# Optimization experiments

Measured on AMD Instinct MI355X. Metric: run time of the kernel, lower is better.

Reference implementation:

```python
import jax, jax.numpy as jnp
import numpy as np
import math

GROUPS = 32
HEADS = 8
EPS = 1e-5


def group_norm(x, w, b):
    B, C, H, W = x.shape
    xg = x.reshape(B, GROUPS, C // GROUPS, H, W)
    mu = xg.mean(axis=(2, 3, 4), keepdims=True)
    var = xg.var(axis=(2, 3, 4), keepdims=True)
    xg = (xg - mu) * jax.lax.rsqrt(var + EPS)
    return xg.reshape(B, C, H, W) * w[None, :, None, None] + b[None, :, None, None]


def setup_inputs() -> dict:
    key = jax.random.key(0)
    ks = jax.random.split(key, 3)
    C = 512
    x = jax.random.normal(ks[0], (4, C, 64, 64), dtype=jnp.float32)
    norm_w = jnp.ones((C,), dtype=jnp.float32)
    norm_b = jnp.zeros((C,), dtype=jnp.float32)
    qkv_w = jax.random.normal(ks[1], (3 * C, C), dtype=jnp.float32) * 0.02
    qkv_b = jnp.zeros((3 * C,), dtype=jnp.float32)
    proj_w = jax.random.normal(ks[2], (C, C), dtype=jnp.float32) * 0.02
    proj_b = jnp.zeros((C,), dtype=jnp.float32)
    return {"x": x, "norm_w": norm_w, "norm_b": norm_b, "qkv_w": qkv_w,
            "qkv_b": qkv_b, "proj_w": proj_w, "proj_b": proj_b}


def reference(x, norm_w, norm_b, qkv_w, qkv_b, proj_w, proj_b):
    B, C, H, W = x.shape
    S = H * W
    head_dim = C // HEADS
    scale = 1.0 / math.sqrt(head_dim)

    h = group_norm(x, norm_w, norm_b)
    # 1x1 conv == pointwise linear over channels
    qkv = jnp.einsum('oc,bchw->bohw', qkv_w, h) + qkv_b[None, :, None, None]
    q, k, v = jnp.split(qkv, 3, axis=1)
    q = q.reshape(B, HEADS, head_dim, S)
    k = k.reshape(B, HEADS, head_dim, S)
    v = v.reshape(B, HEADS, head_dim, S)

    # chunked softmax attention in the original is row-wise softmax, i.e.
    # mathematically identical to full attention over all queries
    attn = jnp.einsum('bhdi,bhdj->bhij', q, k) * scale  # [B,H,S,S]
    attn = jax.nn.softmax(attn, axis=-1)
    out = jnp.einsum('bhij,bhdj->bhdi', attn, v)  # [B,H,d,S]

    out = out.reshape(B, C, H, W)
    out = jnp.einsum('oc,bchw->bohw', proj_w, out) + proj_b[None, :, None, None]
    return out + x
```

## Files before the change

kernel.cpp:

```cpp
#include <hip/hip_runtime.h>
#include <hip/hip_bf16.h>

#define NB 4
#define NC 512
#define NS 4096
#define NH 8
#define HD 64
#define NG 32
#define CPG 16
#define QKC 1024
#define CQF 0.18033688f

typedef __attribute__((ext_vector_type(8))) short bf16x8;
typedef __attribute__((ext_vector_type(4))) float f32x4;
typedef __attribute__((ext_vector_type(16))) float f32x16;

__device__ __forceinline__ unsigned short f2bf(float f) {
  union { float f; unsigned int u; } v; v.f = f;
  unsigned int r = v.u + 0x7FFFu + ((v.u >> 16) & 1u);
  return (unsigned short)(r >> 16);
}

__device__ __forceinline__ unsigned short f2bf_rn(float f) {
  union { __hip_bfloat16 h; unsigned short u; } cv;
  cv.h = __float2bfloat16(f);
  return cv.u;
}

__device__ __forceinline__ void gload16(const unsigned short* g, unsigned short* s) {
  __builtin_amdgcn_global_load_lds(
      (const __attribute__((address_space(1))) unsigned int*)g,
      (__attribute__((address_space(3))) unsigned int*)s, 16, 0, 0);
}

__global__ __launch_bounds__(256) void wprep_k(const float* __restrict__ src,
                                               unsigned short* __restrict__ dst,
                                               int n8, int scale_end8, float scale) {
  int i = blockIdx.x * 256 + threadIdx.x;
  if (i >= n8) return;
  const float4* s = (const float4*)src + (size_t)i * 2;
  float4 a = s[0], b = s[1];
  float sc = (i < scale_end8) ? scale : 1.0f;
  ushort4 u0 = make_ushort4(f2bf_rn(a.x * sc), f2bf_rn(a.y * sc),
                            f2bf_rn(a.z * sc), f2bf_rn(a.w * sc));
  ushort4 u1 = make_ushort4(f2bf_rn(b.x * sc), f2bf_rn(b.y * sc),
                            f2bf_rn(b.z * sc), f2bf_rn(b.w * sc));
  uint4 o;
  o.x = (unsigned)u0.x | ((unsigned)u0.y << 16);
  o.y = (unsigned)u0.z | ((unsigned)u0.w << 16);
  o.z = (unsigned)u1.x | ((unsigned)u1.y << 16);
  o.w = (unsigned)u1.z | ((unsigned)u1.w << 16);
  *((uint4*)dst + i) = o;
}

__global__ __launch_bounds__(256) void gn_stats_k(const float* __restrict__ x,
                                                  float* __restrict__ pstats) {
  int bgq = blockIdx.x;
  const float4* xp = (const float4*)(x + (size_t)bgq * (CPG * NS / 4));
  float s = 0.f, s2 = 0.f;
  #pragma unroll 4
  for (int i = threadIdx.x; i < CPG * NS / 16; i += 256) {
    float4 v = xp[i];
    s  += v.x + v.y + v.z + v.w;
    s2 += v.x * v.x + v.y * v.y + v.z * v.z + v.w * v.w;
  }
  #pragma unroll
  for (int off = 32; off > 0; off >>= 1) {
    s  += __shfl_down(s, off);
    s2 += __shfl_down(s2, off);
  }
  __shared__ float rs[4], rs2[4];
  int wid = threadIdx.x >> 6;
  if ((threadIdx.x & 63) == 0) { rs[wid] = s; rs2[wid] = s2; }
  __syncthreads();
  if (threadIdx.x == 0) {
    pstats[bgq * 2]     = rs[0] + rs[1] + rs[2] + rs[3];
    pstats[bgq * 2 + 1] = rs2[0] + rs2[1] + rs2[2] + rs2[3];
  }
}

__global__ __launch_bounds__(256) void gn_apply_k(const float* __restrict__ x,
                                                  const float* __restrict__ pstats,
                                                  const float* __restrict__ nw,
                                                  const float* __restrict__ nb,
                                                  unsigned short* __restrict__ ht) {
  int st = blockIdx.x, ct = blockIdx.y, b = blockIdx.z;
  int c0 = ct * 64, s0 = st * 64;
  __shared__ unsigned short lds[64][72];
  for (int idx = threadIdx.x; idx < 1024; idx += 256) {
    int row = idx >> 4, c4 = idx & 15;
    int c = c0 + row;
    int gi = (b * NG + (c >> 4)) * 4;
    const float4* pq = (const float4*)(pstats + gi * 2);
    float4 p01 = pq[0], p23 = pq[1];
    float sum = p01.x + p01.z + p23.x + p23.z;
    float ssq = p01.y + p01.w + p23.y + p23.w;
    float inv_n = 1.0f / (CPG * NS);
    float mu = sum * inv_n;
    float var = ssq * inv_n - mu * mu;
    float rstd = rsqrtf(var + 1e-5f);
    float sw = nw[c] * rstd;
    float sb = nb[c] - mu * sw;
    float4 v = *(const float4*)(x + ((size_t)b * NC + c) * NS + s0 + c4 * 4);
    ushort4 u = make_ushort4(f2bf(v.x * sw + sb), f2bf(v.y * sw + sb),
                             f2bf(v.z * sw + sb), f2bf(v.w * sw + sb));
    *(ushort4*)&lds[row][c4 * 4] = u;
  }
  __syncthreads();
  for (int idx = threadIdx.x; idx < 1024; idx += 256) {
    int i = idx >> 4, ch = idx & 15;
    ushort4 u = make_ushort4(lds[ch * 4 + 0][i], lds[ch * 4 + 1][i],
                             lds[ch * 4 + 2][i], lds[ch * 4 + 3][i]);
    *(ushort4*)(ht + ((size_t)b * NS + s0 + i) * NC + c0 + ch * 4) = u;
  }
}

__global__ __launch_bounds__(256) void qkv_gemm_k(const unsigned short* __restrict__ ht,
                                                  const unsigned short* __restrict__ wqb,
                                                  const float* __restrict__ bq,
                                                  unsigned short* __restrict__ qk,
                                                  unsigned short* __restrict__ vt) {
  int b = blockIdx.z;
  int m0 = blockIdx.x * 128, n0 = blockIdx.y * 128;
  __shared__ unsigned short alds[128 * 64];
  __shared__ unsigned short blds[128 * 64];
  const unsigned short* A = ht + (size_t)b * NS * NC;
  int tid = threadIdx.x;
  int l = tid & 63, w = tid >> 6;
  int wr = w >> 1, wc = w & 1;
  int lm = l & 15, lg = l >> 4;
  int lrow = l >> 3, lcb = l & 7;
  f32x4 acc[4][4];
  #pragma unroll
  for (int mi = 0; mi < 4; mi++)
    #pragma unroll
    for (int ni = 0; ni < 4; ni++) acc[mi][ni] = (f32x4){0.f, 0.f, 0.f, 0.f};

  for (int k0 = 0; k0 < NC; k0 += 64) {
    #pragma unroll
    for (int j = 0; j < 4; j++) {
      int row = w * 32 + j * 8 + lrow;
      int scb = lcb ^ (row & 7);
      gload16(A   + (size_t)(m0 + row) * NC + k0 + scb * 8, &alds[(w * 4 + j) * 512]);
      gload16(wqb + (size_t)(n0 + row) * NC + k0 + scb * 8, &blds[(w * 4 + j) * 512]);
    }
    __syncthreads();
    #pragma unroll
    for (int ks = 0; ks < 2; ks++) {
      bf16x8 af[4], bfr[4];
      #pragma unroll
      for (int mi = 0; mi < 4; mi++) {
        int row = wr * 64 + mi * 16 + lm;
        af[mi] = *(const bf16x8*)&alds[((row << 6) + (ks << 5) + (lg << 3)) ^ ((row & 7) << 3)];
      }
      #pragma unroll
      for (int ni = 0; ni < 4; ni++) {
        int row = wc * 64 + ni * 16 + lm;
        bfr[ni] = *(const bf16x8*)&blds[((row << 6) + (ks << 5) + (lg << 3)) ^ ((row & 7) << 3)];
      }
      #pragma unroll
      for (int mi = 0; mi < 4; mi++)
        #pragma unroll
        for (int ni = 0; ni < 4; ni++)
          acc[mi][ni] = __builtin_amdgcn_mfma_f32_16x16x32_bf16(af[mi], bfr[ni], acc[mi][ni], 0, 0, 0);
    }
    __syncthreads();
  }
  if (n0 < QKC) {
    #pragma unroll
    for (int mi = 0; mi < 4; mi++) {
      #pragma unroll
      for (int ni = 0; ni < 4; ni++) {
        int o = n0 + wc * 64 + ni * 16 + lm;
        float bias = bq[o];
        if (o < NC) bias *= CQF;
        #pragma unroll
        for (int q = 0; q < 4; q++) {
          int s = m0 + wr * 64 + mi * 16 + lg * 4 + q;
          qk[((size_t)b * NS + s) * QKC + o] = f2bf(acc[mi][ni][q] + bias);
        }
      }
    }
  } else {
    #pragma unroll
    for (int mi = 0; mi < 4; mi++) {
      int s0 = m0 + wr * 64 + mi * 16 + lg * 4;
      #pragma unroll
      for (int ni = 0; ni < 4; ni++) {
        int o = n0 + wc * 64 + ni * 16 + lm;
        float bias = bq[o];
        int dg = o - QKC;
        ushort4 u = make_ushort4(f2bf(acc[mi][ni][0] + bias), f2bf(acc[mi][ni][1] + bias),
                                 f2bf(acc[mi][ni][2] + bias), f2bf(acc[mi][ni][3] + bias));
        *(ushort4*)(vt + ((size_t)b * NC + dg) * NS + s0) = u;
      }
    }
  }
}

__global__ __launch_bounds__(256) void attn_k(const unsigned short* __restrict__ qk,
                                              const unsigned short* __restrict__ vt,
                                              unsigned short* __restrict__ ob) {
  int qt = blockIdx.x, h = blockIdx.y, b = blockIdx.z;
  int tid = threadIdx.x;
  int l = tid & 63, w = tid >> 6;
  int l31 = l & 31, hi = l >> 5;
  __shared__ unsigned short slds[16384];
  const unsigned short* qkb = qk + (size_t)b * NS * QKC;
  const unsigned short* vtb = vt + ((size_t)b * NC + h * HD) * NS;
  int iw = qt * 128 + w * 32;

  bf16x8 fq[4];
  #pragma unroll
  for (int kk = 0; kk < 4; kk++)
    fq[kk] = *(const bf16x8*)(qkb + (size_t)(iw + l31) * QKC + h * HD + kk * 16 + hi * 8);

  bf16x8 ones;
  #pragma unroll
  for (int e = 0; e < 8; e++) ones[e] = (short)0x3F80;

  int rb = (((l31 << 6) + (hi << 3)) ^ ((l31 & 7) << 3));
  int rbk[4] = { rb, rb ^ 16, rb ^ 32, rb ^ 48 };

  int sr = tid >> 3, sch = (tid & 7) * 8;
  const unsigned short* kp0 = qkb + NC + h * HD + (size_t)sr * QKC + sch;
  const unsigned short* kp1 = kp0 + (size_t)32 * QKC;
  const unsigned short* vp0 = vtb + (size_t)sr * NS + sch;
  const unsigned short* vp1 = vp0 + (size_t)32 * NS;
  int dk0 = (((sr << 6) + sch) ^ ((sr & 7) << 3));
  int dk1 = ((((sr + 32) << 6) + sch) ^ ((sr & 7) << 3));

  f32x16 acc_o0 = {}, acc_o1 = {}, acc_l = {};

  bf16x8 vA[8], vB[8], pA[4], pB[4];
  #pragma unroll
  for (int e = 0; e < 8; e++) vB[e] = (bf16x8){0, 0, 0, 0, 0, 0, 0, 0};
  #pragma unroll
  for (int e = 0; e < 4; e++) pB[e] = (bf16x8){0, 0, 0, 0, 0, 0, 0, 0};

  uint4 rk0 = *(const uint4*)kp0, rk1 = *(const uint4*)kp1;
  uint4 rv0 = *(const uint4*)vp0, rv1 = *(const uint4*)vp1;
  *(uint4*)&slds[dk0] = rk0;        *(uint4*)&slds[dk1] = rk1;
  *(uint4*)&slds[4096 + dk0] = rv0; *(uint4*)&slds[4096 + dk1] = rv1;
  kp0 += (size_t)64 * QKC; kp1 += (size_t)64 * QKC; vp0 += 64; vp1 += 64;
  rk0 = *(const uint4*)kp0; rk1 = *(const uint4*)kp1;
  rv0 = *(const uint4*)vp0; rv1 = *(const uint4*)vp1;
  __syncthreads();

  #define CVTSW(SA, q, DST) {                                                       \
    unsigned X0, X1, Y0, Y1;                                                        \
    asm("v_cvt_pk_bf16_f32 %0, %1, %2" : "=v"(X0) : "v"(SA[q*8+0]), "v"(SA[q*8+1]));\
    asm("v_cvt_pk_bf16_f32 %0, %1, %2" : "=v"(X1) : "v"(SA[q*8+2]), "v"(SA[q*8+3]));\
    asm("v_cvt_pk_bf16_f32 %0, %1, %2" : "=v"(Y0) : "v"(SA[q*8+4]), "v"(SA[q*8+5]));\
    asm("v_cvt_pk_bf16_f32 %0, %1, %2" : "=v"(Y1) : "v"(SA[q*8+6]), "v"(SA[q*8+7]));\
    asm("v_permlane32_swap_b32 %0, %1" : "+v"(X0), "+v"(Y0));                       \
    asm("v_permlane32_swap_b32 %0, %1" : "+v"(X1), "+v"(Y1));                       \
    union { unsigned u[4]; bf16x8 v; } pu = {{X0, X1, Y0, Y1}};                     \
    DST = pu.v; }

  #define TILE(BUF, t, VN, VP, PN, PP) {                                            \
    *(uint4*)&slds[(BUF^1)*8192 + dk0] = rk0;                                       \
    *(uint4*)&slds[(BUF^1)*8192 + dk1] = rk1;                                       \
    *(uint4*)&slds[(BUF^1)*8192 + 4096 + dk0] = rv0;                                \
    *(uint4*)&slds[(BUF^1)*8192 + 4096 + dk1] = rv1;                                \
    if ((t) + 2 < 64) {                                                             \
      kp0 += (size_t)64 * QKC; kp1 += (size_t)64 * QKC; vp0 += 64; vp1 += 64;       \
      rk0 = *(const uint4*)kp0; rk1 = *(const uint4*)kp1;                           \
      rv0 = *(const uint4*)vp0; rv1 = *(const uint4*)vp1;                           \
    }                                                                               \
    const unsigned short* Kr = &slds[(BUF)*8192];                                   \
    const unsigned short* Vr = &slds[(BUF)*8192 + 4096];                            \
    f32x16 sa0 = {}, sa1 = {};                                                      \
    __builtin_amdgcn_s_setprio(1);                                                  \
    _Pragma("unroll")                                                               \
    for (int kk = 0; kk < 4; kk++) {                                                \
      bf16x8 ak = *(const bf16x8*)&Kr[rbk[kk]];                                     \
      sa0 = __builtin_amdgcn_mfma_f32_32x32x16_bf16(ak, fq[kk], sa0, 0, 0, 0);      \
    }                                                                               \
    _Pragma("unroll")                                                               \
    for (int kk = 0; kk < 4; kk++) {                                                \
      bf16x8 ak = *(const bf16x8*)&Kr[rbk[kk] + 2048];                              \
      sa1 = __builtin_amdgcn_mfma_f32_32x32x16_bf16(ak, fq[kk], sa1, 0, 0, 0);      \
    }                                                                               \
    _Pragma("unroll")                                                               \
    for (int kk = 0; kk < 4; kk++) {                                                \
      VN[kk]     = *(const bf16x8*)&Vr[rbk[kk]];                                    \
      VN[kk + 4] = *(const bf16x8*)&Vr[rbk[kk] + 2048];                             \
    }                                                                               \
    _Pragma("unroll")                                                               \
    for (int bq_ = 0; bq_ < 4; bq_++) {                                             \
      acc_l  = __builtin_amdgcn_mfma_f32_32x32x16_bf16(PP[bq_], ones, acc_l, 0, 0, 0);        \
      acc_o0 = __builtin_amdgcn_mfma_f32_32x32x16_bf16(PP[bq_], VP[bq_], acc_o0, 0, 0, 0);    \
      acc_o1 = __builtin_amdgcn_mfma_f32_32x32x16_bf16(PP[bq_], VP[bq_ + 4], acc_o1, 0, 0, 0);\
    }                                                                               \
    __builtin_amdgcn_s_setprio(0);                                                  \
    _Pragma("unroll")                                                               \
    for (int r = 0; r < 16; r++) {                                                  \
      sa0[r] = __builtin_amdgcn_exp2f(sa0[r]);                                      \
      sa1[r] = __builtin_amdgcn_exp2f(sa1[r]);                                      \
    }                                                                               \
    CVTSW(sa0, 0, PN[0]);                                                           \
    CVTSW(sa0, 1, PN[1]);                                                           \
    CVTSW(sa1, 0, PN[2]);                                                           \
    CVTSW(sa1, 1, PN[3]);                                                           \
    __syncthreads(); }

  for (int t = 0; t < 64; t += 2) {
    TILE(0, t,     vA, vB, pA, pB)
    TILE(1, t + 1, vB, vA, pB, pA)
  }
  #undef TILE
  #undef CVTSW

  #pragma unroll
  for (int bq_ = 0; bq_ < 4; bq_++) {
    acc_l  = __builtin_amdgcn_mfma_f32_32x32x16_bf16(pB[bq_], ones, acc_l, 0, 0, 0);
    acc_o0 = __builtin_amdgcn_mfma_f32_32x32x16_bf16(pB[bq_], vB[bq_], acc_o0, 0, 0, 0);
    acc_o1 = __builtin_amdgcn_mfma_f32_32x32x16_bf16(pB[bq_], vB[bq_ + 4], acc_o1, 0, 0, 0);
  }

  #pragma unroll
  for (int r = 0; r < 16; r++) {
    float inv = __builtin_amdgcn_rcpf(acc_l[r]);
    int i = (r & 3) + 8 * (r >> 2) + 4 * hi;
    size_t rowo = ((size_t)b * NS + (iw + i)) * NC + h * HD;
    ob[rowo + l31]      = f2bf_rn(acc_o0[r] * inv);
    ob[rowo + 32 + l31] = f2bf_rn(acc_o1[r] * inv);
  }
}

__global__ __launch_bounds__(256) void proj_gemm_k(const unsigned short* __restrict__ wpb,
                                                   const float* __restrict__ bp,
                                                   const unsigned short* __restrict__ obuf,
                                                   const float* __restrict__ x,
                                                   float* __restrict__ out) {
  int b = blockIdx.z;
  int m0 = blockIdx.x * 128, n0 = blockIdx.y * 128;
  __shared__ unsigned short alds[128 * 64];
  __shared__ unsigned short blds[128 * 64];
  const unsigned short* Bt = obuf + (size_t)b * NS * NC;
  int tid = threadIdx.x;
  int l = tid & 63, w = tid >> 6;
  int wr = w >> 1, wc = w & 1;
  int lm = l & 15, lg = l >> 4;
  int lrow = l >> 3, lcb = l & 7;
  f32x4 acc[4][4];
  #pragma unroll
  for (int mi = 0; mi < 4; mi++)
    #pragma unroll
    for (int ni = 0; ni < 4; ni++) acc[mi][ni] = (f32x4){0.f, 0.f, 0.f, 0.f};

  for (int k0 = 0; k0 < NC; k0 += 64) {
    #pragma unroll
    for (int j = 0; j < 4; j++) {
      int row = w * 32 + j * 8 + lrow;
      int scb = lcb ^ (row & 7);
      gload16(wpb + (size_t)(m0 + row) * NC + k0 + scb * 8, &alds[(w * 4 + j) * 512]);
      gload16(Bt  + (size_t)(n0 + row) * NC + k0 + scb * 8, &blds[(w * 4 + j) * 512]);
    }
    __syncthreads();
    #pragma unroll
    for (int ks = 0; ks < 2; ks++) {
      bf16x8 af[4], bfr[4];
      #pragma unroll
      for (int mi = 0; mi < 4; mi++) {
        int row = wr * 64 + mi * 16 + lm;
        af[mi] = *(const bf16x8*)&alds[((row << 6) + (ks << 5) + (lg << 3)) ^ ((row & 7) << 3)];
      }
      #pragma unroll
      for (int ni = 0; ni < 4; ni++) {
        int row = wc * 64 + ni * 16 + lm;
        bfr[ni] = *(const bf16x8*)&blds[((row << 6) + (ks << 5) + (lg << 3)) ^ ((row & 7) << 3)];
      }
      #pragma unroll
      for (int mi = 0; mi < 4; mi++)
        #pragma unroll
        for (int ni = 0; ni < 4; ni++)
          acc[mi][ni] = __builtin_amdgcn_mfma_f32_16x16x32_bf16(af[mi], bfr[ni], acc[mi][ni], 0, 0, 0);
    }
    __syncthreads();
  }
  #pragma unroll
  for (int mi = 0; mi < 4; mi++) {
    #pragma unroll
    for (int q = 0; q < 4; q++) {
      int o = m0 + wr * 64 + mi * 16 + lg * 4 + q;
      float bias = bp[o];
      #pragma unroll
      for (int ni = 0; ni < 4; ni++) {
        int s = n0 + wc * 64 + ni * 16 + lm;
        size_t idx = ((size_t)b * NC + o) * NS + s;
        out[idx] = acc[mi][ni][q] + bias + x[idx];
      }
    }
  }
}

extern "C" void kernel_launch(void* const* d_in, const int* in_sizes, int n_in,
                              void* d_out, int out_size, void* d_ws, size_t ws_size,
                              hipStream_t stream) {
  const float* x  = (const float*)d_in[0];
  const float* nw = (const float*)d_in[1];
  const float* nb = (const float*)d_in[2];
  const float* wq = (const float*)d_in[3];
  const float* bq = (const float*)d_in[4];
  const float* wp = (const float*)d_in[5];
  const float* bp = (const float*)d_in[6];
  float* out = (float*)d_out;

  char* ws = (char*)d_ws;
  size_t off = 0;
  off += 1024;
  unsigned short* ht  = (unsigned short*)(ws + off); off += (size_t)NB * NS * NC * 2;
  unsigned short* qk  = (unsigned short*)(ws + off); off += (size_t)NB * NS * QKC * 2;
  unsigned short* vt  = (unsigned short*)(ws + off); off += (size_t)NB * NS * NC * 2;
  unsigned short* wqb = (unsigned short*)(ws + off); off += (size_t)3 * NC * NC * 2;
  unsigned short* wpb = (unsigned short*)(ws + off); off += (size_t)NC * NC * 2;
  unsigned short* ob  = ht;
  float* pstats = (float*)qk;

  wprep_k<<<dim3((3 * NC * NC / 8 + 255) / 256), 256, 0, stream>>>(
      wq, wqb, 3 * NC * NC / 8, NC * NC / 8, CQF);
  wprep_k<<<dim3((NC * NC / 8 + 255) / 256), 256, 0, stream>>>(
      wp, wpb, NC * NC / 8, 0, 1.0f);
  gn_stats_k<<<dim3(NB * NG * 4), 256, 0, stream>>>(x, pstats);
  gn_apply_k<<<dim3(NS / 64, NC / 64, NB), 256, 0, stream>>>(x, pstats, nw, nb, ht);
  qkv_gemm_k<<<dim3(NS / 128, 1536 / 128, NB), 256, 0, stream>>>(ht, wqb, bq, qk, vt);
  attn_k<<<dim3(NS / 128, NH, NB), 256, 0, stream>>>(qk, vt, ob);
  proj_gemm_k<<<dim3(NC / 128, NS / 128, NB), 256, 0, stream>>>(wpb, bp, ob, x, out);
}
```

Measured before the change: 248.1 us.

## Restructure attention loop to overlap next-tile QK MFMA with previous-tile exp and PV

```diff
diff --git a/kernel.cpp b/kernel.cpp
--- a/kernel.cpp
+++ b/kernel.cpp
@@ -231,12 +231,8 @@
   int dk1 = ((((sr + 32) << 6) + sch) ^ ((sr & 7) << 3));
 
   f32x16 acc_o0 = {}, acc_o1 = {}, acc_l = {};
-
-  bf16x8 vA[8], vB[8], pA[4], pB[4];
-  #pragma unroll
-  for (int e = 0; e < 8; e++) vB[e] = (bf16x8){0, 0, 0, 0, 0, 0, 0, 0};
-  #pragma unroll
-  for (int e = 0; e < 4; e++) pB[e] = (bf16x8){0, 0, 0, 0, 0, 0, 0, 0};
+  f32x16 saA0, saA1, saB0, saB1;
+  bf16x8 vA[8], vB[8];
 
   uint4 rk0 = *(const uint4*)kp0, rk1 = *(const uint4*)kp1;
   uint4 rv0 = *(const uint4*)vp0, rv1 = *(const uint4*)vp1;
@@ -247,22 +243,51 @@
   rv0 = *(const uint4*)vp0; rv1 = *(const uint4*)vp1;
   __syncthreads();
 
-  #define CVTSW(SA, q, DST) {                                                       \
+  {
+    *(uint4*)&slds[8192 + dk0] = rk0;        *(uint4*)&slds[8192 + dk1] = rk1;
+    *(uint4*)&slds[8192 + 4096 + dk0] = rv0; *(uint4*)&slds[8192 + 4096 + dk1] = rv1;
+    kp0 += (size_t)64 * QKC; kp1 += (size_t)64 * QKC; vp0 += 64; vp1 += 64;
+    rk0 = *(const uint4*)kp0; rk1 = *(const uint4*)kp1;
+    rv0 = *(const uint4*)vp0; rv1 = *(const uint4*)vp1;
+    saA0 = (f32x16){}; saA1 = (f32x16){};
+    __builtin_amdgcn_s_setprio(1);
+    #pragma unroll
+    for (int kk = 0; kk < 4; kk++) {
+      bf16x8 ak = *(const bf16x8*)&slds[rbk[kk]];
+      saA0 = __builtin_amdgcn_mfma_f32_32x32x16_bf16(ak, fq[kk], saA0, 0, 0, 0);
+    }
+    #pragma unroll
+    for (int kk = 0; kk < 4; kk++) {
+      bf16x8 ak = *(const bf16x8*)&slds[rbk[kk] + 2048];
+      saA1 = __builtin_amdgcn_mfma_f32_32x32x16_bf16(ak, fq[kk], saA1, 0, 0, 0);
+    }
+    __builtin_amdgcn_s_setprio(0);
+    #pragma unroll
+    for (int kk = 0; kk < 4; kk++) {
+      vA[kk]     = *(const bf16x8*)&slds[4096 + rbk[kk]];
+      vA[kk + 4] = *(const bf16x8*)&slds[4096 + rbk[kk] + 2048];
+    }
+    __syncthreads();
+  }
+
+  #define CVTSW(S0, q, DST) {                                                       \
     unsigned X0, X1, Y0, Y1;                                                        \
-    asm("v_cvt_pk_bf16_f32 %0, %1, %2" : "=v"(X0) : "v"(SA[q*8+0]), "v"(SA[q*8+1]));\
-    asm("v_cvt_pk_bf16_f32 %0, %1, %2" : "=v"(X1) : "v"(SA[q*8+2]), "v"(SA[q*8+3]));\
-    asm("v_cvt_pk_bf16_f32 %0, %1, %2" : "=v"(Y0) : "v"(SA[q*8+4]), "v"(SA[q*8+5]));\
-    asm("v_cvt_pk_bf16_f32 %0, %1, %2" : "=v"(Y1) : "v"(SA[q*8+6]), "v"(SA[q*8+7]));\
+    asm("v_cvt_pk_bf16_f32 %0, %1, %2" : "=v"(X0) : "v"(S0[q*8+0]), "v"(S0[q*8+1]));\
+    asm("v_cvt_pk_bf16_f32 %0, %1, %2" : "=v"(X1) : "v"(S0[q*8+2]), "v"(S0[q*8+3]));\
+    asm("v_cvt_pk_bf16_f32 %0, %1, %2" : "=v"(Y0) : "v"(S0[q*8+4]), "v"(S0[q*8+5]));\
+    asm("v_cvt_pk_bf16_f32 %0, %1, %2" : "=v"(Y1) : "v"(S0[q*8+6]), "v"(S0[q*8+7]));\
     asm("v_permlane32_swap_b32 %0, %1" : "+v"(X0), "+v"(Y0));                       \
     asm("v_permlane32_swap_b32 %0, %1" : "+v"(X1), "+v"(Y1));                       \
     union { unsigned u[4]; bf16x8 v; } pu = {{X0, X1, Y0, Y1}};                     \
     DST = pu.v; }
 
-  #define TILE(BUF, t, VN, VP, PN, PP) {                                            \
-    *(uint4*)&slds[(BUF^1)*8192 + dk0] = rk0;                                       \
-    *(uint4*)&slds[(BUF^1)*8192 + dk1] = rk1;                                       \
-    *(uint4*)&slds[(BUF^1)*8192 + 4096 + dk0] = rv0;                                \
-    *(uint4*)&slds[(BUF^1)*8192 + 4096 + dk1] = rv1;                                \
+  #define ROUND(BUF, t, SAN0, SAN1, SAP0, SAP1, VN, VP) {                           \
+    if ((t) + 1 < 64) {                                                             \
+      *(uint4*)&slds[(BUF^1)*8192 + dk0] = rk0;                                     \
+      *(uint4*)&slds[(BUF^1)*8192 + dk1] = rk1;                                     \
+      *(uint4*)&slds[(BUF^1)*8192 + 4096 + dk0] = rv0;                              \
+      *(uint4*)&slds[(BUF^1)*8192 + 4096 + dk1] = rv1;                              \
+    }                                                                               \
     if ((t) + 2 < 64) {                                                             \
       kp0 += (size_t)64 * QKC; kp1 += (size_t)64 * QKC; vp0 += 64; vp1 += 64;       \
       rk0 = *(const uint4*)kp0; rk1 = *(const uint4*)kp1;                           \
@@ -270,54 +295,83 @@
     }                                                                               \
     const unsigned short* Kr = &slds[(BUF)*8192];                                   \
     const unsigned short* Vr = &slds[(BUF)*8192 + 4096];                            \
-    f32x16 sa0 = {}, sa1 = {};                                                      \
+    SAN0 = (f32x16){}; SAN1 = (f32x16){};                                           \
     __builtin_amdgcn_s_setprio(1);                                                  \
     _Pragma("unroll")                                                               \
     for (int kk = 0; kk < 4; kk++) {                                                \
       bf16x8 ak = *(const bf16x8*)&Kr[rbk[kk]];                                     \
-      sa0 = __builtin_amdgcn_mfma_f32_32x32x16_bf16(ak, fq[kk], sa0, 0, 0, 0);      \
+      SAN0 = __builtin_amdgcn_mfma_f32_32x32x16_bf16(ak, fq[kk], SAN0, 0, 0, 0);    \
     }                                                                               \
     _Pragma("unroll")                                                               \
     for (int kk = 0; kk < 4; kk++) {                                                \
       bf16x8 ak = *(const bf16x8*)&Kr[rbk[kk] + 2048];                              \
-      sa1 = __builtin_amdgcn_mfma_f32_32x32x16_bf16(ak, fq[kk], sa1, 0, 0, 0);      \
+      SAN1 = __builtin_amdgcn_mfma_f32_32x32x16_bf16(ak, fq[kk], SAN1, 0, 0, 0);    \
+    }                                                                               \
+    __builtin_amdgcn_s_setprio(0);                                                  \
+           \
+    _Pragma("unroll")                                                               \
+    for (int r = 0; r < 16; r++) {                                                  \
+      SAP0[r] = __builtin_amdgcn_exp2f(SAP0[r]);                                    \
+      SAP1[r] = __builtin_amdgcn_exp2f(SAP1[r]);                                    \
     }                                                                               \
     _Pragma("unroll")                                                               \
     for (int kk = 0; kk < 4; kk++) {                                                \
       VN[kk]     = *(const bf16x8*)&Vr[rbk[kk]];                                    \
       VN[kk + 4] = *(const bf16x8*)&Vr[rbk[kk] + 2048];                             \
     }                                                                               \
-    _Pragma("unroll")                                                               \
-    for (int bq_ = 0; bq_ < 4; bq_++) {                                             \
-      acc_l  = __builtin_amdgcn_mfma_f32_32x32x16_bf16(PP[bq_], ones, acc_l, 0, 0, 0);        \
-      acc_o0 = __builtin_amdgcn_mfma_f32_32x32x16_bf16(PP[bq_], VP[bq_], acc_o0, 0, 0, 0);    \
-      acc_o1 = __builtin_amdgcn_mfma_f32_32x32x16_bf16(PP[bq_], VP[bq_ + 4], acc_o1, 0, 0, 0);\
-    }                                                                               \
+    bf16x8 p0_, p1_, p2_, p3_;                                                      \
+    CVTSW(SAP0, 0, p0_);                                                            \
+    CVTSW(SAP0, 1, p1_);                                                            \
+    CVTSW(SAP1, 0, p2_);                                                            \
+    CVTSW(SAP1, 1, p3_);                                                            \
+    __builtin_amdgcn_s_setprio(1);                                                  \
+    acc_l  = __builtin_amdgcn_mfma_f32_32x32x16_bf16(p0_, ones, acc_l, 0, 0, 0);    \
+    acc_o0 = __builtin_amdgcn_mfma_f32_32x32x16_bf16(p0_, VP[0], acc_o0, 0, 0, 0);  \
+    acc_o1 = __builtin_amdgcn_mfma_f32_32x32x16_bf16(p0_, VP[4], acc_o1, 0, 0, 0);  \
+    acc_l  = __builtin_amdgcn_mfma_f32_32x32x16_bf16(p1_, ones, acc_l, 0, 0, 0);    \
+    acc_o0 = __builtin_amdgcn_mfma_f32_32x32x16_bf16(p1_, VP[1], acc_o0, 0, 0, 0);  \
+    acc_o1 = __builtin_amdgcn_mfma_f32_32x32x16_bf16(p1_, VP[5], acc_o1, 0, 0, 0);  \
+    acc_l  = __builtin_amdgcn_mfma_f32_32x32x16_bf16(p2_, ones, acc_l, 0, 0, 0);    \
+    acc_o0 = __builtin_amdgcn_mfma_f32_32x32x16_bf16(p2_, VP[2], acc_o0, 0, 0, 0);  \
+    acc_o1 = __builtin_amdgcn_mfma_f32_32x32x16_bf16(p2_, VP[6], acc_o1, 0, 0, 0);  \
+    acc_l  = __builtin_amdgcn_mfma_f32_32x32x16_bf16(p3_, ones, acc_l, 0, 0, 0);    \
+    acc_o0 = __builtin_amdgcn_mfma_f32_32x32x16_bf16(p3_, VP[3], acc_o0, 0, 0, 0);  \
+    acc_o1 = __builtin_amdgcn_mfma_f32_32x32x16_bf16(p3_, VP[7], acc_o1, 0, 0, 0);  \
     __builtin_amdgcn_s_setprio(0);                                                  \
-    _Pragma("unroll")                                                               \
-    for (int r = 0; r < 16; r++) {                                                  \
-      sa0[r] = __builtin_amdgcn_exp2f(sa0[r]);                                      \
-      sa1[r] = __builtin_amdgcn_exp2f(sa1[r]);                                      \
-    }                                                                               \
-    CVTSW(sa0, 0, PN[0]);                                                           \
-    CVTSW(sa0, 1, PN[1]);                                                           \
-    CVTSW(sa1, 0, PN[2]);                                                           \
-    CVTSW(sa1, 1, PN[3]);                                                           \
     __syncthreads(); }
 
-  for (int t = 0; t < 64; t += 2) {
-    TILE(0, t,     vA, vB, pA, pB)
-    TILE(1, t + 1, vB, vA, pB, pA)
-  }
-  #undef TILE
+  for (int t = 1; t < 63; t += 2) {
+    ROUND(1, t,     saB0, saB1, saA0, saA1, vB, vA)
+    ROUND(0, t + 1, saA0, saA1, saB0, saB1, vA, vB)
+  }
+  ROUND(1, 63, saB0, saB1, saA0, saA1, vB, vA)
+  #undef ROUND
+
+  {
+    #pragma unroll
+    for (int r = 0; r < 16; r++) {
+      saB0[r] = __builtin_amdgcn_exp2f(saB0[r]);
+      saB1[r] = __builtin_amdgcn_exp2f(saB1[r]);
+    }
+    bf16x8 p0_, p1_, p2_, p3_;
+    CVTSW(saB0, 0, p0_);
+    CVTSW(saB0, 1, p1_);
+    CVTSW(saB1, 0, p2_);
+    CVTSW(saB1, 1, p3_);
+    acc_l  = __builtin_amdgcn_mfma_f32_32x32x16_bf16(p0_, ones, acc_l, 0, 0, 0);
+    acc_o0 = __builtin_amdgcn_mfma_f32_32x32x16_bf16(p0_, vB[0], acc_o0, 0, 0, 0);
+    acc_o1 = __builtin_amdgcn_mfma_f32_32x32x16_bf16(p0_, vB[4], acc_o1, 0, 0, 0);
+    acc_l  = __builtin_amdgcn_mfma_f32_32x32x16_bf16(p1_, ones, acc_l, 0, 0, 0);
+    acc_o0 = __builtin_amdgcn_mfma_f32_32x32x16_bf16(p1_, vB[1], acc_o0, 0, 0, 0);
+    acc_o1 = __builtin_amdgcn_mfma_f32_32x32x16_bf16(p1_, vB[5], acc_o1, 0, 0, 0);
+    acc_l  = __builtin_amdgcn_mfma_f32_32x32x16_bf16(p2_, ones, acc_l, 0, 0, 0);
+    acc_o0 = __builtin_amdgcn_mfma_f32_32x32x16_bf16(p2_, vB[2], acc_o0, 0, 0, 0);
+    acc_o1 = __builtin_amdgcn_mfma_f32_32x32x16_bf16(p2_, vB[6], acc_o1, 0, 0, 0);
+    acc_l  = __builtin_amdgcn_mfma_f32_32x32x16_bf16(p3_, ones, acc_l, 0, 0, 0);
+    acc_o0 = __builtin_amdgcn_mfma_f32_32x32x16_bf16(p3_, vB[3], acc_o0, 0, 0, 0);
+    acc_o1 = __builtin_amdgcn_mfma_f32_32x32x16_bf16(p3_, vB[7], acc_o1, 0, 0, 0);
+  }
   #undef CVTSW
-
-  #pragma unroll
-  for (int bq_ = 0; bq_ < 4; bq_++) {
-    acc_l  = __builtin_amdgcn_mfma_f32_32x32x16_bf16(pB[bq_], ones, acc_l, 0, 0, 0);
-    acc_o0 = __builtin_amdgcn_mfma_f32_32x32x16_bf16(pB[bq_], vB[bq_], acc_o0, 0, 0, 0);
-    acc_o1 = __builtin_amdgcn_mfma_f32_32x32x16_bf16(pB[bq_], vB[bq_ + 4], acc_o1, 0, 0, 0);
-  }
 
   #pragma unroll
   for (int r = 0; r < 16; r++) {
```

Result: no change. 249.3 us (+0.5%).
